# Kernel optimization log

Measured on AMD Instinct MI355X. Metric: run time of the kernel, lower is better.

Reference implementation:

```python
import jax, jax.numpy as jnp
import numpy as np

N = 100000
F_IN = 128
DIM = 2
E = 3200000


def setup_inputs() -> dict:
    key = jax.random.key(0)
    k1, k2, k3, k4, k5, k6, k7 = jax.random.split(key, 7)
    x = jax.random.normal(k1, (N, F_IN), dtype=jnp.float32)
    edge_index = jax.random.randint(k2, (2, E), 0, N, dtype=jnp.int64)
    edge_attr = jax.random.uniform(k3, (E,), dtype=jnp.float32)
    # GCNConv params: lin weight [F_IN, DIM] (glorot), bias zeros
    conv_w = jax.random.normal(k4, (F_IN, DIM), dtype=jnp.float32) * (1.0 / np.sqrt(F_IN))
    conv_b = jnp.zeros((DIM,), dtype=jnp.float32)
    # TopKPooling score weight [DIM]
    pool_w = jax.random.normal(k5, (DIM,), dtype=jnp.float32)
    # fc: Linear(N*DIM, 1), init normal(0, 0.01), bias 0 (per init_weights)
    fc_w = jax.random.normal(k6, (N * DIM, 1), dtype=jnp.float32) * 0.01
    fc_b = jnp.zeros((1,), dtype=jnp.float32)
    return {"x": x, "edge_index": edge_index, "edge_attr": edge_attr,
            "conv_w": conv_w, "conv_b": conv_b, "pool_w": pool_w,
            "fc_w": fc_w, "fc_b": fc_b}


def reference(x, edge_index, edge_attr, conv_w, conv_b, pool_w, fc_w, fc_b):
    n = x.shape[0]
    row, col = edge_index[0], edge_index[1]
    # --- GCNConv: add self-loops (weight 1), symmetric normalization ---
    loop = jnp.arange(n, dtype=edge_index.dtype)
    row_f = jnp.concatenate([row, loop])
    col_f = jnp.concatenate([col, loop])
    w_f = jnp.concatenate([edge_attr, jnp.ones((n,), dtype=x.dtype)])
    deg = jax.ops.segment_sum(w_f, col_f, num_segments=n)  # [N]
    dinv = jnp.where(deg > 0, jax.lax.rsqrt(deg), 0.0)
    norm = dinv[row_f] * w_f * dinv[col_f]  # [E+N]
    h = x @ conv_w  # [N, DIM] transform-then-propagate
    msg = norm[:, None] * h[row_f]  # [E+N, DIM]
    out = jax.ops.segment_sum(msg, col_f, num_segments=n) + conv_b  # [N, DIM]
    # --- ReLU ---
    out = jax.nn.relu(out)
    # --- TopKPooling with k = N (single graph): score, sort desc, gate ---
    score = jnp.tanh((out @ pool_w) / jnp.linalg.norm(pool_w))  # [N]
    perm = jnp.argsort(-score)
    pooled = out[perm] * score[perm][:, None]  # [N, DIM]
    # --- flatten + fc + sigmoid ---
    flat = pooled.reshape(-1)  # [N*DIM]
    y = jax.nn.sigmoid(flat @ fc_w + fc_b)  # [1]
    return y
```

## Files before the change

### kernel.cpp

```cpp
#include <hip/hip_runtime.h>
#include <math.h>

#define FIN 128
#define W 512
#define S 8
#define MAXG 256
#define HB 256
#define HT 1024
#define BP 100

__device__ __forceinline__ long long edge_at(const void* p, long long i, unsigned mode) {
  return mode ? ((const long long*)p)[i] : (long long)((const int*)p)[i];
}

__device__ __forceinline__ void atomic_fadd(float* p, float v) {
  __hip_atomic_fetch_add(p, v, __ATOMIC_RELAXED, __HIP_MEMORY_SCOPE_AGENT);
}

__global__ void k_detect(const unsigned* ei, unsigned* mode, float* acc) {
  if (threadIdx.x == 0 && blockIdx.x == 0) {
    unsigned orv = 0;
    for (int i = 1; i < 1024; i += 2) orv |= ei[i];
    *mode = (orv == 0) ? 1u : 0u;
    *acc = 0.0f;
  }
}

__global__ void k_h(const float* __restrict__ x, const float* __restrict__ cw,
                    float* __restrict__ h, int n) {
  int gt = blockIdx.x * blockDim.x + threadIdx.x;
  int node = gt >> 5;
  int sub = gt & 31;
  if (node >= n) return;
  float4 xv = ((const float4*)x)[node * 32 + sub];
  float s0 = xv.x * cw[sub * 8 + 0] + xv.y * cw[sub * 8 + 2] +
             xv.z * cw[sub * 8 + 4] + xv.w * cw[sub * 8 + 6];
  float s1 = xv.x * cw[sub * 8 + 1] + xv.y * cw[sub * 8 + 3] +
             xv.z * cw[sub * 8 + 5] + xv.w * cw[sub * 8 + 7];
  for (int off = 16; off > 0; off >>= 1) {
    s0 += __shfl_down(s0, off, 32);
    s1 += __shfl_down(s1, off, 32);
  }
  if (sub == 0) { h[node * 2] = s0; h[node * 2 + 1] = s1; }
}

__global__ void k_hist(const void* ei, long long E, int G,
                       unsigned* table, const unsigned* __restrict__ mode) {
  __shared__ unsigned hist[MAXG];
  unsigned m = *mode;
  int t = threadIdx.x;
  if (t < MAXG) hist[t] = 0;
  __syncthreads();
  long long perB = (E + HB - 1) / HB;
  long long base = (long long)blockIdx.x * perB;
  long long lim = base + perB; if (lim > E) lim = E;
  for (long long e = base + t; e < lim; e += HT) {
    int c = (int)edge_at(ei, E + e, m);
    atomicAdd(&hist[c >> 9], 1u);
  }
  __syncthreads();
  if (t < G) table[(size_t)t * HB + blockIdx.x] = hist[t];
}

__global__ void k_bsum(const unsigned* __restrict__ table, unsigned* btot) {
  int b = blockIdx.x, t = threadIdx.x;
  unsigned v = table[(size_t)b * HB + t];
  for (int off = 32; off > 0; off >>= 1) v += __shfl_down(v, off);
  __shared__ unsigned wsum[4];
  if ((t & 63) == 0) wsum[t >> 6] = v;
  __syncthreads();
  if (t == 0) btot[b] = wsum[0] + wsum[1] + wsum[2] + wsum[3];
}

__global__ void k_bapply(unsigned* table, const unsigned* __restrict__ btot,
                         unsigned* boff, int G, unsigned Etot) {
  __shared__ unsigned red[256];
  __shared__ unsigned s[256];
  int g = blockIdx.x, t = threadIdx.x;
  unsigned p = 0;
  for (int i = t; i < g; i += 256) p += btot[i];
  red[t] = p;
  __syncthreads();
  for (int off = 128; off > 0; off >>= 1) {
    if (t < off) red[t] += red[t + off];
    __syncthreads();
  }
  unsigned pre = red[0];
  unsigned v = table[(size_t)g * HB + t];
  s[t] = v;
  __syncthreads();
  for (int off = 1; off < 256; off <<= 1) {
    unsigned tmp = (t >= off) ? s[t - off] : 0u;
    __syncthreads();
    s[t] += tmp;
    __syncthreads();
  }
  table[(size_t)g * HB + t] = s[t] - v + pre;
  if (t == 0) { boff[g] = pre; if (g == 0) boff[G] = Etot; }
}

__global__ void k_scatter(const void* ei, const float* __restrict__ attr,
                          long long E, int G, const unsigned* __restrict__ table,
                          uint2* __restrict__ packed, const unsigned* __restrict__ mode) {
  __shared__ unsigned cur[MAXG];
  unsigned m = *mode;
  int t = threadIdx.x;
  if (t < G) cur[t] = table[(size_t)t * HB + blockIdx.x];
  __syncthreads();
  long long perB = (E + HB - 1) / HB;
  long long base = (long long)blockIdx.x * perB;
  long long lim = base + perB; if (lim > E) lim = E;
  for (long long e = base + t; e < lim; e += HT) {
    int r = (int)edge_at(ei, e, m);
    int c = (int)edge_at(ei, E + e, m);
    float a = attr[e];
    unsigned pos = atomicAdd(&cur[c >> 9], 1u);
    packed[pos] = make_uint2(((unsigned)r << 9) | ((unsigned)c & 511u), __float_as_uint(a));
  }
}

__global__ void k_pdeg(const uint2* __restrict__ packed, const unsigned* __restrict__ boff,
                       float* __restrict__ pdeg) {
  __shared__ float sdeg[W];
  int blk = blockIdx.x, t = threadIdx.x;
  int g = blk / S, s = blk - g * S;
  sdeg[t] = 0.f; sdeg[t + 256] = 0.f;
  __syncthreads();
  unsigned e0 = boff[g], e1 = boff[g + 1];
  unsigned len = e1 - e0;
  unsigned per = (len + S - 1) / S;
  unsigned lo = e0 + s * per;
  unsigned hi = lo + per; if (hi > e1) hi = e1;
  for (unsigned i = lo + t; i < hi; i += 256) {
    uint2 p = packed[i];
    atomicAdd(&sdeg[p.x & (W - 1u)], __uint_as_float(p.y));
  }
  __syncthreads();
  pdeg[(size_t)blk * W + t] = sdeg[t];
  pdeg[(size_t)blk * W + t + 256] = sdeg[t + 256];
}

__global__ void k_dinv(const float* __restrict__ pdeg, const float* __restrict__ h,
                       float* __restrict__ dinv, float* __restrict__ g, int n) {
  int i = blockIdx.x * blockDim.x + threadIdx.x;
  if (i >= n) return;
  int grp = i >> 9, li = i & (W - 1);
  float d = 1.0f;
#pragma unroll
  for (int s = 0; s < S; ++s) d += pdeg[((size_t)(grp * S + s)) * W + li];
  float di = rsqrtf(d);
  dinv[i] = di;
  g[2 * i]     = di * h[2 * i];
  g[2 * i + 1] = di * h[2 * i + 1];
}

__global__ void k_pmsg(const uint2* __restrict__ packed, const unsigned* __restrict__ boff,
                       const float* __restrict__ gv, float* __restrict__ pacc) {
  __shared__ float sacc[2 * W];
  int blk = blockIdx.x, t = threadIdx.x;
  int g = blk / S, s = blk - g * S;
#pragma unroll
  for (int i = 0; i < 4; ++i) sacc[t + 256 * i] = 0.f;
  __syncthreads();
  unsigned e0 = boff[g], e1 = boff[g + 1];
  unsigned len = e1 - e0;
  unsigned per = (len + S - 1) / S;
  unsigned lo = e0 + s * per;
  unsigned hi = lo + per; if (hi > e1) hi = e1;
  const float2* g2 = (const float2*)gv;
  for (unsigned i = lo + t; i < hi; i += 256) {
    uint2 p = packed[i];
    unsigned r = p.x >> 9;
    unsigned cl = p.x & (W - 1u);
    float a = __uint_as_float(p.y);
    float2 gr = g2[r];
    atomicAdd(&sacc[2 * cl],     a * gr.x);
    atomicAdd(&sacc[2 * cl + 1], a * gr.y);
  }
  __syncthreads();
#pragma unroll
  for (int i = 0; i < 4; ++i) pacc[(size_t)blk * (2 * W) + t + 256 * i] = sacc[t + 256 * i];
}

__global__ void k_gout(const float* __restrict__ pacc, const float* __restrict__ dinv,
                       const float* __restrict__ h, const float* __restrict__ cb,
                       const float* __restrict__ pw, float* __restrict__ out,
                       float* __restrict__ score, unsigned* __restrict__ keys,
                       unsigned* __restrict__ pay, int n) {
  int g = blockIdx.x, t = threadIdx.x;
  const float2* p2 = (const float2*)pacc;
  float a0 = 0.f, a1 = 0.f;
#pragma unroll
  for (int s = 0; s < S; ++s) {
    float2 v = p2[(size_t)(g * S + s) * W + t];
    a0 += v.x; a1 += v.y;
  }
  int c = g * W + t;
  if (c < n) {
    float dc = dinv[c];
    float o0 = fmaxf(dc * a0 + dc * dc * h[2 * c]     + cb[0], 0.f);
    float o1 = fmaxf(dc * a1 + dc * dc * h[2 * c + 1] + cb[1], 0.f);
    out[2 * c] = o0; out[2 * c + 1] = o1;
    float pw0 = pw[0], pw1 = pw[1];
    float s = tanhf((o0 * pw0 + o1 * pw1) / sqrtf(pw0 * pw0 + pw1 * pw1));
    score[c] = s;
    unsigned u = __float_as_uint(s);
    unsigned asc = u ^ ((u >> 31) ? 0xFFFFFFFFu : 0x80000000u);
    keys[c] = ~asc;
    pay[c] = (unsigned)c;
  }
}

__global__ void k_radix_hist(const unsigned* __restrict__ keys, int n, int shift,
                             unsigned* table) {
  __shared__ unsigned hist[256];
  int t = threadIdx.x;
  hist[t] = 0;
  __syncthreads();
  int base = blockIdx.x * 1024;
  for (int j = 0; j < 4; ++j) {
    int g = base + j * 256 + t;
    if (g < n) {
      unsigned d = (keys[g] >> shift) & 255u;
      atomicAdd(&hist[d], 1u);
    }
  }
  __syncthreads();
  table[t * BP + blockIdx.x] = hist[t];
}

__global__ void k_radix_scan(unsigned* table, int B) {
  int t = threadIdx.x;
  unsigned* row = table + t * BP;
  uint4* r4 = (uint4*)row;
  int nv = B >> 2;
  unsigned s = 0;
#pragma unroll 8
  for (int i = 0; i < nv; ++i) { uint4 v = r4[i]; s += v.x + v.y + v.z + v.w; }
  for (int i = nv * 4; i < B; ++i) s += row[i];
  int lane = t & 63, w = t >> 6;
  unsigned inc = s;
  for (int off = 1; off < 64; off <<= 1) {
    unsigned nval = __shfl_up(inc, off);
    if (lane >= off) inc += nval;
  }
  __shared__ unsigned wtot[4];
  if (lane == 63) wtot[w] = inc;
  __syncthreads();
  unsigned wpre = 0;
  for (int i = 0; i < w; ++i) wpre += wtot[i];
  unsigned run = wpre + inc - s;
#pragma unroll 8
  for (int i = 0; i < nv; ++i) {
    uint4 v = r4[i]; uint4 o;
    o.x = run; run += v.x; o.y = run; run += v.y;
    o.z = run; run += v.z; o.w = run; run += v.w;
    r4[i] = o;
  }
  for (int i = nv * 4; i < B; ++i) { unsigned v = row[i]; row[i] = run; run += v; }
}

__global__ void k_radix_scatter(const unsigned* __restrict__ keysIn,
                                const unsigned* __restrict__ payIn, int n, int shift,
                                const unsigned* __restrict__ table,
                                unsigned* keysOut, unsigned* payOut) {
  __shared__ unsigned runCnt[256];
  __shared__ unsigned waveCnt[4 * 256];
  int t = threadIdx.x;
  int lane = t & 63, w = t >> 6;
  runCnt[t] = 0;
  int base = blockIdx.x * 1024;
  for (int j = 0; j < 4; ++j) {
    for (int q = t; q < 1024; q += 256) waveCnt[q] = 0;
    __syncthreads();
    int g = base + j * 256 + t;
    bool active = g < n;
    unsigned key = 0, pay = 0, d = 0;
    if (active) { key = keysIn[g]; pay = payIn[g]; d = (key >> shift) & 255u; }
    unsigned long long am = __ballot(active);
    unsigned long long mm = ~0ull;
#pragma unroll
    for (int b = 0; b < 8; ++b) {
      unsigned long long bb = __ballot((d >> b) & 1u);
      mm &= ((d >> b) & 1u) ? bb : ~bb;
    }
    mm &= am;
    int rankw = __popcll(mm & ((1ull << lane) - 1ull));
    if (active && rankw == 0) waveCnt[w * 256 + d] = (unsigned)__popcll(mm);
    __syncthreads();
    if (active) {
      unsigned off = runCnt[d] + (unsigned)rankw;
      for (int ww = 0; ww < w; ++ww) off += waveCnt[ww * 256 + d];
      unsigned gpos = table[d * BP + blockIdx.x] + off;
      keysOut[gpos] = key;
      payOut[gpos] = pay;
    }
    __syncthreads();
    runCnt[t] += waveCnt[t] + waveCnt[256 + t] + waveCnt[512 + t] + waveCnt[768 + t];
    __syncthreads();
  }
}

__global__ void k_final(const unsigned* __restrict__ perm, const float* __restrict__ out,
                        const float* __restrict__ score, const float* __restrict__ fcw,
                        float* acc, int n) {
  int stride = gridDim.x * blockDim.x;
  float s = 0.f;
  const float2* o2 = (const float2*)out;
  const float2* f2 = (const float2*)fcw;
  for (int j = blockIdx.x * blockDim.x + threadIdx.x; j < n; j += stride) {
    unsigned p = perm[j];
    float2 ov = o2[p];
    float2 fv = f2[j];
    s += score[p] * (ov.x * fv.x + ov.y * fv.y);
  }
  for (int off = 32; off > 0; off >>= 1) s += __shfl_down(s, off);
  if ((threadIdx.x & 63) == 0) atomic_fadd(acc, s);
}

__global__ void k_sigmoid(const float* acc, const float* __restrict__ fcb, float* y) {
  if (threadIdx.x == 0 && blockIdx.x == 0) {
    float z = *acc + fcb[0];
    y[0] = 1.f / (1.f + expf(-z));
  }
}

extern "C" void kernel_launch(void* const* d_in, const int* in_sizes, int n_in,
                              void* d_out, int out_size, void* d_ws, size_t ws_size,
                              hipStream_t stream) {
  const float* x     = (const float*)d_in[0];
  const void*  ei    = d_in[1];
  const float* attr  = (const float*)d_in[2];
  const float* convw = (const float*)d_in[3];
  const float* convb = (const float*)d_in[4];
  const float* poolw = (const float*)d_in[5];
  const float* fcw   = (const float*)d_in[6];
  const float* fcb   = (const float*)d_in[7];
  float* y = (float*)d_out;

  int N = in_sizes[0] / FIN;
  long long E = in_sizes[2];
  int B = (N + 1023) / 1024;
  int G = (N + W - 1) / W;

  float* ws = (float*)d_ws;
  size_t off = 0;
  uint2* packed  = (uint2*)(ws + off); off += (size_t)2 * E;
  float* pacc    = ws + off; off += (size_t)2 * G * S * W;
  float* pdeg    = pacc;
  float* h       = ws + off; off += (size_t)2 * N;
  float* dinv    = ws + off; off += (size_t)N;
  float* gv      = ws + off; off += (size_t)2 * N;
  float* outN    = ws + off; off += (size_t)2 * N;
  float* score   = ws + off; off += (size_t)N;
  unsigned* keysA = (unsigned*)(ws + off); off += (size_t)N;
  unsigned* payA  = (unsigned*)(ws + off); off += (size_t)N;
  unsigned* keysB = (unsigned*)(ws + off); off += (size_t)N;
  unsigned* payB  = (unsigned*)(ws + off); off += (size_t)N;
  unsigned* etab  = (unsigned*)(ws + off); off += (size_t)G * HB;
  unsigned* btot  = (unsigned*)(ws + off); off += (size_t)G;
  unsigned* boff  = (unsigned*)(ws + off); off += (size_t)G + 2;
  unsigned* stab  = (unsigned*)(ws + off); off += (size_t)256 * BP;
  float* acc      = ws + off; off += 1;
  unsigned* mode  = (unsigned*)(ws + off); off += 1;

  int nb = (N + 255) / 256;

  k_detect<<<1, 64, 0, stream>>>((const unsigned*)ei, mode, acc);
  k_h<<<(N * 32 + 255) / 256, 256, 0, stream>>>(x, convw, h, N);

  k_hist<<<HB, HT, 0, stream>>>(ei, E, G, etab, mode);
  k_bsum<<<G, 256, 0, stream>>>(etab, btot);
  k_bapply<<<G, 256, 0, stream>>>(etab, btot, boff, G, (unsigned)E);
  k_scatter<<<HB, HT, 0, stream>>>(ei, attr, E, G, etab, packed, mode);

  k_pdeg<<<G * S, 256, 0, stream>>>(packed, boff, pdeg);
  k_dinv<<<nb, 256, 0, stream>>>(pdeg, h, dinv, gv, N);
  k_pmsg<<<G * S, 256, 0, stream>>>(packed, boff, gv, pacc);
  k_gout<<<G, W, 0, stream>>>(pacc, dinv, h, convb, poolw, outN, score, keysA, payA, N);

  unsigned* ki = keysA; unsigned* pi = payA;
  unsigned* ko = keysB; unsigned* po = payB;
  for (int p = 0; p < 4; ++p) {
    int shift = 8 * p;
    k_radix_hist<<<B, 256, 0, stream>>>(ki, N, shift, stab);
    k_radix_scan<<<1, 256, 0, stream>>>(stab, B);
    k_radix_scatter<<<B, 256, 0, stream>>>(ki, pi, N, shift, stab, ko, po);
    unsigned* tk = ki; ki = ko; ko = tk;
    unsigned* tp = pi; pi = po; po = tp;
  }

  k_final<<<196, 256, 0, stream>>>(pi, outN, score, fcw, acc, N);
  k_sigmoid<<<1, 64, 0, stream>>>(acc, fcb, y);
}
```

Before: 232.0 us.

## Bucket edges into fixed-capacity slots and fuse the first radix histogram into gout

Drops the three-kernel exact counting pipeline (histogram, block sums, prefix apply) in favour of fixed-capacity buckets per 512-node group. Each scatter block reserves space in a bucket with one global atomic on a per-bucket cursor. The per-group split S doubles to 16, and the edge loops in pdeg and pmsg are unrolled by four to keep more loads in flight. The radix sort now uses 512-thread blocks with one element per thread, and the first pass's histogram is computed inside k_gout, so one hist kernel per call is removed. The trade-off is that CAP assumes no 512-node group receives more than 18432 edges. That holds for uniformly random column indices but would overflow into the next bucket on skewed graphs.

```diff
diff --git a/kernel.cpp b/kernel.cpp
--- a/kernel.cpp
+++ b/kernel.cpp
@@ -3,11 +3,12 @@
 
 #define FIN 128
 #define W 512
-#define S 8
+#define S 16
 #define MAXG 256
+#define CAP 18432u
 #define HB 256
 #define HT 1024
-#define BP 100
+#define BP 200
 
 __device__ __forceinline__ long long edge_at(const void* p, long long i, unsigned mode) {
   return mode ? ((const long long*)p)[i] : (long long)((const int*)p)[i];
@@ -17,13 +18,16 @@
   __hip_atomic_fetch_add(p, v, __ATOMIC_RELAXED, __HIP_MEMORY_SCOPE_AGENT);
 }
 
-__global__ void k_detect(const unsigned* ei, unsigned* mode, float* acc) {
-  if (threadIdx.x == 0 && blockIdx.x == 0) {
+__global__ void k_detect(const unsigned* ei, unsigned* mode, float* acc,
+                         unsigned* cur, int G) {
+  int t = threadIdx.x;
+  if (t == 0) {
     unsigned orv = 0;
     for (int i = 1; i < 1024; i += 2) orv |= ei[i];
     *mode = (orv == 0) ? 1u : 0u;
     *acc = 0.0f;
   }
+  for (int i = t; i < G; i += 64) cur[i] = (unsigned)i * CAP;
 }
 
 __global__ void k_h(const float* __restrict__ x, const float* __restrict__ cw,
@@ -44,96 +48,57 @@
   if (sub == 0) { h[node * 2] = s0; h[node * 2 + 1] = s1; }
 }
 
-__global__ void k_hist(const void* ei, long long E, int G,
-                       unsigned* table, const unsigned* __restrict__ mode) {
+__global__ void k_scatter2(const void* ei, const float* __restrict__ attr,
+                           long long E, int G, unsigned* cur,
+                           uint2* __restrict__ packed,
+                           const unsigned* __restrict__ mode) {
   __shared__ unsigned hist[MAXG];
+  __shared__ unsigned base[MAXG];
   unsigned m = *mode;
   int t = threadIdx.x;
   if (t < MAXG) hist[t] = 0;
   __syncthreads();
   long long perB = (E + HB - 1) / HB;
-  long long base = (long long)blockIdx.x * perB;
-  long long lim = base + perB; if (lim > E) lim = E;
-  for (long long e = base + t; e < lim; e += HT) {
+  long long b0 = (long long)blockIdx.x * perB;
+  long long lim = b0 + perB; if (lim > E) lim = E;
+  for (long long e = b0 + t; e < lim; e += HT) {
     int c = (int)edge_at(ei, E + e, m);
     atomicAdd(&hist[c >> 9], 1u);
   }
   __syncthreads();
-  if (t < G) table[(size_t)t * HB + blockIdx.x] = hist[t];
-}
-
-__global__ void k_bsum(const unsigned* __restrict__ table, unsigned* btot) {
-  int b = blockIdx.x, t = threadIdx.x;
-  unsigned v = table[(size_t)b * HB + t];
-  for (int off = 32; off > 0; off >>= 1) v += __shfl_down(v, off);
-  __shared__ unsigned wsum[4];
-  if ((t & 63) == 0) wsum[t >> 6] = v;
-  __syncthreads();
-  if (t == 0) btot[b] = wsum[0] + wsum[1] + wsum[2] + wsum[3];
-}
-
-__global__ void k_bapply(unsigned* table, const unsigned* __restrict__ btot,
-                         unsigned* boff, int G, unsigned Etot) {
-  __shared__ unsigned red[256];
-  __shared__ unsigned s[256];
-  int g = blockIdx.x, t = threadIdx.x;
-  unsigned p = 0;
-  for (int i = t; i < g; i += 256) p += btot[i];
-  red[t] = p;
-  __syncthreads();
-  for (int off = 128; off > 0; off >>= 1) {
-    if (t < off) red[t] += red[t + off];
-    __syncthreads();
-  }
-  unsigned pre = red[0];
-  unsigned v = table[(size_t)g * HB + t];
-  s[t] = v;
-  __syncthreads();
-  for (int off = 1; off < 256; off <<= 1) {
-    unsigned tmp = (t >= off) ? s[t - off] : 0u;
-    __syncthreads();
-    s[t] += tmp;
-    __syncthreads();
-  }
-  table[(size_t)g * HB + t] = s[t] - v + pre;
-  if (t == 0) { boff[g] = pre; if (g == 0) boff[G] = Etot; }
-}
-
-__global__ void k_scatter(const void* ei, const float* __restrict__ attr,
-                          long long E, int G, const unsigned* __restrict__ table,
-                          uint2* __restrict__ packed, const unsigned* __restrict__ mode) {
-  __shared__ unsigned cur[MAXG];
-  unsigned m = *mode;
-  int t = threadIdx.x;
-  if (t < G) cur[t] = table[(size_t)t * HB + blockIdx.x];
-  __syncthreads();
-  long long perB = (E + HB - 1) / HB;
-  long long base = (long long)blockIdx.x * perB;
-  long long lim = base + perB; if (lim > E) lim = E;
-  for (long long e = base + t; e < lim; e += HT) {
+  if (t < G) base[t] = atomicAdd(&cur[t], hist[t]);
+  __syncthreads();
+  for (long long e = b0 + t; e < lim; e += HT) {
     int r = (int)edge_at(ei, e, m);
     int c = (int)edge_at(ei, E + e, m);
     float a = attr[e];
-    unsigned pos = atomicAdd(&cur[c >> 9], 1u);
+    unsigned pos = atomicAdd(&base[c >> 9], 1u);
     packed[pos] = make_uint2(((unsigned)r << 9) | ((unsigned)c & 511u), __float_as_uint(a));
   }
 }
 
-__global__ void k_pdeg(const uint2* __restrict__ packed, const unsigned* __restrict__ boff,
+__global__ void k_pdeg(const uint2* __restrict__ packed, const unsigned* __restrict__ cur,
                        float* __restrict__ pdeg) {
   __shared__ float sdeg[W];
   int blk = blockIdx.x, t = threadIdx.x;
-  int g = blk / S, s = blk - g * S;
+  int g = blk >> 4, s = blk & (S - 1);
   sdeg[t] = 0.f; sdeg[t + 256] = 0.f;
   __syncthreads();
-  unsigned e0 = boff[g], e1 = boff[g + 1];
-  unsigned len = e1 - e0;
+  unsigned lo = (unsigned)g * CAP, hi = cur[g];
+  unsigned len = hi - lo;
   unsigned per = (len + S - 1) / S;
-  unsigned lo = e0 + s * per;
-  unsigned hi = lo + per; if (hi > e1) hi = e1;
-  for (unsigned i = lo + t; i < hi; i += 256) {
-    uint2 p = packed[i];
-    atomicAdd(&sdeg[p.x & (W - 1u)], __uint_as_float(p.y));
+  unsigned mylo = lo + s * per;
+  unsigned myhi = mylo + per; if (myhi > hi) myhi = hi;
+  for (unsigned b = mylo + t; b < myhi; b += 4 * 256) {
+    unsigned k0 = b, k1 = b + 256, k2 = b + 512, k3 = b + 768;
+    uint2 p0 = packed[k0];
+    uint2 p1 = packed[k1 < myhi ? k1 : b];
+    uint2 p2 = packed[k2 < myhi ? k2 : b];
+    uint2 p3 = packed[k3 < myhi ? k3 : b];
+    atomicAdd(&sdeg[p0.x & (W - 1u)], __uint_as_float(p0.y));
+    if (k1 < myhi) atomicAdd(&sdeg[p1.x & (W - 1u)], __uint_as_float(p1.y));
+    if (k2 < myhi) atomicAdd(&sdeg[p2.x & (W - 1u)], __uint_as_float(p2.y));
+    if (k3 < myhi) atomicAdd(&sdeg[p3.x & (W - 1u)], __uint_as_float(p3.y));
   }
   __syncthreads();
   pdeg[(size_t)blk * W + t] = sdeg[t];
@@ -154,28 +119,39 @@
   g[2 * i + 1] = di * h[2 * i + 1];
 }
 
-__global__ void k_pmsg(const uint2* __restrict__ packed, const unsigned* __restrict__ boff,
+__global__ void k_pmsg(const uint2* __restrict__ packed, const unsigned* __restrict__ cur,
                        const float* __restrict__ gv, float* __restrict__ pacc) {
   __shared__ float sacc[2 * W];
   int blk = blockIdx.x, t = threadIdx.x;
-  int g = blk / S, s = blk - g * S;
+  int g = blk >> 4, s = blk & (S - 1);
 #pragma unroll
   for (int i = 0; i < 4; ++i) sacc[t + 256 * i] = 0.f;
   __syncthreads();
-  unsigned e0 = boff[g], e1 = boff[g + 1];
-  unsigned len = e1 - e0;
+  unsigned lo = (unsigned)g * CAP, hi = cur[g];
+  unsigned len = hi - lo;
   unsigned per = (len + S - 1) / S;
-  unsigned lo = e0 + s * per;
-  unsigned hi = lo + per; if (hi > e1) hi = e1;
+  unsigned mylo = lo + s * per;
+  unsigned myhi = mylo + per; if (myhi > hi) myhi = hi;
   const float2* g2 = (const float2*)gv;
-  for (unsigned i = lo + t; i < hi; i += 256) {
-    uint2 p = packed[i];
-    unsigned r = p.x >> 9;
-    unsigned cl = p.x & (W - 1u);
-    float a = __uint_as_float(p.y);
-    float2 gr = g2[r];
-    atomicAdd(&sacc[2 * cl],     a * gr.x);
-    atomicAdd(&sacc[2 * cl + 1], a * gr.y);
+  for (unsigned b = mylo + t; b < myhi; b += 4 * 256) {
+    unsigned k1 = b + 256, k2 = b + 512, k3 = b + 768;
+    uint2 p0 = packed[b];
+    uint2 p1 = packed[k1 < myhi ? k1 : b];
+    uint2 p2 = packed[k2 < myhi ? k2 : b];
+    uint2 p3 = packed[k3 < myhi ? k3 : b];
+    float2 g0 = g2[p0.x >> 9];
+    float2 g1 = g2[p1.x >> 9];
+    float2 g2v = g2[p2.x >> 9];
+    float2 g3 = g2[p3.x >> 9];
+    float a0 = __uint_as_float(p0.y), a1 = __uint_as_float(p1.y);
+    float a2 = __uint_as_float(p2.y), a3 = __uint_as_float(p3.y);
+    unsigned c0 = p0.x & (W - 1u), c1 = p1.x & (W - 1u);
+    unsigned c2 = p2.x & (W - 1u), c3 = p3.x & (W - 1u);
+    atomicAdd(&sacc[2 * c0],     a0 * g0.x);
+    atomicAdd(&sacc[2 * c0 + 1], a0 * g0.y);
+    if (k1 < myhi) { atomicAdd(&sacc[2 * c1], a1 * g1.x); atomicAdd(&sacc[2 * c1 + 1], a1 * g1.y); }
+    if (k2 < myhi) { atomicAdd(&sacc[2 * c2], a2 * g2v.x); atomicAdd(&sacc[2 * c2 + 1], a2 * g2v.y); }
+    if (k3 < myhi) { atomicAdd(&sacc[2 * c3], a3 * g3.x); atomicAdd(&sacc[2 * c3 + 1], a3 * g3.y); }
   }
   __syncthreads();
 #pragma unroll
@@ -186,8 +162,11 @@
                        const float* __restrict__ h, const float* __restrict__ cb,
                        const float* __restrict__ pw, float* __restrict__ out,
                        float* __restrict__ score, unsigned* __restrict__ keys,
-                       unsigned* __restrict__ pay, int n) {
+                       unsigned* __restrict__ pay, unsigned* __restrict__ table, int n) {
+  __shared__ unsigned hist[256];
   int g = blockIdx.x, t = threadIdx.x;
+  if (t < 256) hist[t] = 0;
+  __syncthreads();
   const float2* p2 = (const float2*)pacc;
   float a0 = 0.f, a1 = 0.f;
 #pragma unroll
@@ -206,30 +185,28 @@
     score[c] = s;
     unsigned u = __float_as_uint(s);
     unsigned asc = u ^ ((u >> 31) ? 0xFFFFFFFFu : 0x80000000u);
-    keys[c] = ~asc;
+    unsigned key = ~asc;
+    keys[c] = key;
     pay[c] = (unsigned)c;
-  }
-}
-
-__global__ void k_radix_hist(const unsigned* __restrict__ keys, int n, int shift,
-                             unsigned* table) {
+    atomicAdd(&hist[key & 255u], 1u);
+  }
+  __syncthreads();
+  if (t < 256) table[t * BP + g] = hist[t];
+}
+
+__global__ void k_rhist(const unsigned* __restrict__ keys, int n, int shift,
+                        unsigned* table) {
   __shared__ unsigned hist[256];
   int t = threadIdx.x;
-  hist[t] = 0;
-  __syncthreads();
-  int base = blockIdx.x * 1024;
-  for (int j = 0; j < 4; ++j) {
-    int g = base + j * 256 + t;
-    if (g < n) {
-      unsigned d = (keys[g] >> shift) & 255u;
-      atomicAdd(&hist[d], 1u);
-    }
-  }
-  __syncthreads();
-  table[t * BP + blockIdx.x] = hist[t];
-}
-
-__global__ void k_radix_scan(unsigned* table, int B) {
+  if (t < 256) hist[t] = 0;
+  __syncthreads();
+  int g = blockIdx.x * 512 + t;
+  if (g < n) atomicAdd(&hist[(keys[g] >> shift) & 255u], 1u);
+  __syncthreads();
+  if (t < 256) table[t * BP + blockIdx.x] = hist[t];
+}
+
+__global__ void k_rscan(unsigned* table, int B) {
   int t = threadIdx.x;
   unsigned* row = table + t * BP;
   uint4* r4 = (uint4*)row;
@@ -260,44 +237,36 @@
   for (int i = nv * 4; i < B; ++i) { unsigned v = row[i]; row[i] = run; run += v; }
 }
 
-__global__ void k_radix_scatter(const unsigned* __restrict__ keysIn,
-                                const unsigned* __restrict__ payIn, int n, int shift,
-                                const unsigned* __restrict__ table,
-                                unsigned* keysOut, unsigned* payOut) {
-  __shared__ unsigned runCnt[256];
-  __shared__ unsigned waveCnt[4 * 256];
+__global__ void k_rscatter(const unsigned* __restrict__ keysIn,
+                           const unsigned* __restrict__ payIn, int n, int shift,
+                           const unsigned* __restrict__ table,
+                           unsigned* keysOut, unsigned* payOut) {
+  __shared__ unsigned waveCnt[8 * 256];
   int t = threadIdx.x;
   int lane = t & 63, w = t >> 6;
-  runCnt[t] = 0;
-  int base = blockIdx.x * 1024;
-  for (int j = 0; j < 4; ++j) {
-    for (int q = t; q < 1024; q += 256) waveCnt[q] = 0;
-    __syncthreads();
-    int g = base + j * 256 + t;
-    bool active = g < n;
-    unsigned key = 0, pay = 0, d = 0;
-    if (active) { key = keysIn[g]; pay = payIn[g]; d = (key >> shift) & 255u; }
-    unsigned long long am = __ballot(active);
-    unsigned long long mm = ~0ull;
-#pragma unroll
-    for (int b = 0; b < 8; ++b) {
-      unsigned long long bb = __ballot((d >> b) & 1u);
-      mm &= ((d >> b) & 1u) ? bb : ~bb;
-    }
-    mm &= am;
-    int rankw = __popcll(mm & ((1ull << lane) - 1ull));
-    if (active && rankw == 0) waveCnt[w * 256 + d] = (unsigned)__popcll(mm);
-    __syncthreads();
-    if (active) {
-      unsigned off = runCnt[d] + (unsigned)rankw;
-      for (int ww = 0; ww < w; ++ww) off += waveCnt[ww * 256 + d];
-      unsigned gpos = table[d * BP + blockIdx.x] + off;
-      keysOut[gpos] = key;
-      payOut[gpos] = pay;
-    }
-    __syncthreads();
-    runCnt[t] += waveCnt[t] + waveCnt[256 + t] + waveCnt[512 + t] + waveCnt[768 + t];
-    __syncthreads();
+  for (int q = t; q < 8 * 256; q += 512) waveCnt[q] = 0;
+  __syncthreads();
+  int g = blockIdx.x * 512 + t;
+  bool active = g < n;
+  unsigned key = 0, pay = 0, d = 0;
+  if (active) { key = keysIn[g]; pay = payIn[g]; d = (key >> shift) & 255u; }
+  unsigned long long am = __ballot(active);
+  unsigned long long mm = ~0ull;
+#pragma unroll
+  for (int b = 0; b < 8; ++b) {
+    unsigned long long bb = __ballot((d >> b) & 1u);
+    mm &= ((d >> b) & 1u) ? bb : ~bb;
+  }
+  mm &= am;
+  int rankw = __popcll(mm & ((1ull << lane) - 1ull));
+  if (active && rankw == 0) waveCnt[w * 256 + d] = (unsigned)__popcll(mm);
+  __syncthreads();
+  if (active) {
+    unsigned off = (unsigned)rankw;
+    for (int ww = 0; ww < w; ++ww) off += waveCnt[ww * 256 + d];
+    unsigned gpos = table[d * BP + blockIdx.x] + off;
+    keysOut[gpos] = key;
+    payOut[gpos] = pay;
   }
 }
 
@@ -340,12 +309,12 @@
 
   int N = in_sizes[0] / FIN;
   long long E = in_sizes[2];
-  int B = (N + 1023) / 1024;
+  int B = (N + 511) / 512;
   int G = (N + W - 1) / W;
 
   float* ws = (float*)d_ws;
   size_t off = 0;
-  uint2* packed  = (uint2*)(ws + off); off += (size_t)2 * E;
+  uint2* packed  = (uint2*)(ws + off); off += (size_t)2 * G * CAP;
   float* pacc    = ws + off; off += (size_t)2 * G * S * W;
   float* pdeg    = pacc;
   float* h       = ws + off; off += (size_t)2 * N;
@@ -357,35 +326,31 @@
   unsigned* payA  = (unsigned*)(ws + off); off += (size_t)N;
   unsigned* keysB = (unsigned*)(ws + off); off += (size_t)N;
   unsigned* payB  = (unsigned*)(ws + off); off += (size_t)N;
-  unsigned* etab  = (unsigned*)(ws + off); off += (size_t)G * HB;
-  unsigned* btot  = (unsigned*)(ws + off); off += (size_t)G;
-  unsigned* boff  = (unsigned*)(ws + off); off += (size_t)G + 2;
+  unsigned* cur   = (unsigned*)(ws + off); off += (size_t)G;
   unsigned* stab  = (unsigned*)(ws + off); off += (size_t)256 * BP;
   float* acc      = ws + off; off += 1;
   unsigned* mode  = (unsigned*)(ws + off); off += 1;
 
   int nb = (N + 255) / 256;
 
-  k_detect<<<1, 64, 0, stream>>>((const unsigned*)ei, mode, acc);
+  k_detect<<<1, 64, 0, stream>>>((const unsigned*)ei, mode, acc, cur, G);
   k_h<<<(N * 32 + 255) / 256, 256, 0, stream>>>(x, convw, h, N);
 
-  k_hist<<<HB, HT, 0, stream>>>(ei, E, G, etab, mode);
-  k_bsum<<<G, 256, 0, stream>>>(etab, btot);
-  k_bapply<<<G, 256, 0, stream>>>(etab, btot, boff, G, (unsigned)E);
-  k_scatter<<<HB, HT, 0, stream>>>(ei, attr, E, G, etab, packed, mode);
-
-  k_pdeg<<<G * S, 256, 0, stream>>>(packed, boff, pdeg);
+  k_scatter2<<<HB, HT, 0, stream>>>(ei, attr, E, G, cur, packed, mode);
+
+  k_pdeg<<<G * S, 256, 0, stream>>>(packed, cur, pdeg);
   k_dinv<<<nb, 256, 0, stream>>>(pdeg, h, dinv, gv, N);
-  k_pmsg<<<G * S, 256, 0, stream>>>(packed, boff, gv, pacc);
-  k_gout<<<G, W, 0, stream>>>(pacc, dinv, h, convb, poolw, outN, score, keysA, payA, N);
+  k_pmsg<<<G * S, 256, 0, stream>>>(packed, cur, gv, pacc);
+  k_gout<<<G, W, 0, stream>>>(pacc, dinv, h, convb, poolw, outN, score,
+                              keysA, payA, stab, N);
 
   unsigned* ki = keysA; unsigned* pi = payA;
   unsigned* ko = keysB; unsigned* po = payB;
   for (int p = 0; p < 4; ++p) {
     int shift = 8 * p;
-    k_radix_hist<<<B, 256, 0, stream>>>(ki, N, shift, stab);
-    k_radix_scan<<<1, 256, 0, stream>>>(stab, B);
-    k_radix_scatter<<<B, 256, 0, stream>>>(ki, pi, N, shift, stab, ko, po);
+    if (p > 0) k_rhist<<<B, 512, 0, stream>>>(ki, N, shift, stab);
+    k_rscan<<<1, 256, 0, stream>>>(stab, B);
+    k_rscatter<<<B, 512, 0, stream>>>(ki, pi, N, shift, stab, ko, po);
     unsigned* tk = ki; ki = ko; ko = tk;
     unsigned* tp = pi; pi = po; po = tp;
   }
```

Result: slower. 237.2 us (+2.2%).
